# Kernel optimization log

Hardware: AMD Instinct MI355X
Metric: run time of the kernel (lower is better)

The kernel has to match this reference:

```python
import jax, jax.numpy as jnp
import numpy as np


def _conv1x1(x, W, b):
    # x: [B,C,H,W], W: [O,C], b: [O]  -> [B,O,H,W]
    return jnp.einsum('bchw,oc->bohw', x, W) + b[None, :, None, None]


def setup_inputs() -> dict:
    key = jax.random.key(0)
    ks = jax.random.split(key, 8)
    B, C, H, W = 16, 512, 48, 48
    d = C // 8
    scale = 0.02
    return {
        'feat_map': jax.random.normal(ks[0], (B, C, H, W), dtype=jnp.float32),
        'Wq': jax.random.normal(ks[1], (d, C), dtype=jnp.float32) * scale,
        'bq': jax.random.normal(ks[2], (d,), dtype=jnp.float32) * scale,
        'Wk': jax.random.normal(ks[3], (d, C), dtype=jnp.float32) * scale,
        'bk': jax.random.normal(ks[4], (d,), dtype=jnp.float32) * scale,
        'Wv': jax.random.normal(ks[5], (C, C), dtype=jnp.float32) * scale,
        'bv': jax.random.normal(ks[6], (C,), dtype=jnp.float32) * scale,
        'gamma': jnp.ones((1,), dtype=jnp.float32),
    }


def reference(feat_map, Wq, bq, Wk, bk, Wv, bv, gamma):
    # SAModule (DANet spatial attention):
    #   q = conv1(x) -> [B, d, HW] -> permute [B, HW, d]
    #   k = conv2(x) -> [B, d, HW]
    #   attn = softmax(q @ k, axis=-1)            # [B, HW, HW]
    #   v = conv3(x) -> [B, C, HW]
    #   out = v @ attn^T -> [B, C, H, W]
    #   y = gamma * out + x
    B, C, H, W = feat_map.shape
    HW = H * W
    q = _conv1x1(feat_map, Wq, bq).reshape(B, -1, HW).transpose(0, 2, 1)  # [B,HW,d]
    k = _conv1x1(feat_map, Wk, bk).reshape(B, -1, HW)                     # [B,d,HW]
    attn = jax.nn.softmax(jnp.einsum('bnd,bdm->bnm', q, k), axis=-1)      # [B,HW,HW]
    v = _conv1x1(feat_map, Wv, bv).reshape(B, C, HW)                      # [B,C,HW]
    out = jnp.einsum('bcm,bnm->bcn', v, attn).reshape(B, C, H, W)
    return gamma * out + feat_map
```

## Files before the change

kernel.cpp:

```cpp
#include <hip/hip_runtime.h>

typedef __bf16 bf16x8 __attribute__((ext_vector_type(8)));
typedef __bf16 bf16x4 __attribute__((ext_vector_type(4)));
typedef float  f32x4  __attribute__((ext_vector_type(4)));

constexpr int kHW = 2304;
constexpr int kC  = 512;

#if __has_builtin(__builtin_amdgcn_exp2f)
#define EXP2(x) __builtin_amdgcn_exp2f(x)
#else
#define EXP2(x) exp2f(x)
#endif

__device__ __forceinline__ void dma16(const __bf16* g, __bf16* l) {
    __builtin_amdgcn_global_load_lds(
        (const volatile __attribute__((address_space(1))) void*)g,
        (volatile __attribute__((address_space(3))) void*)l, 16, 0, 0);
}

__global__ void pack_weights(const float* __restrict__ Wq, const float* __restrict__ Wk,
                             const float* __restrict__ Wv, __bf16* __restrict__ Wqk2,
                             __bf16* __restrict__ Wvb2) {
    int idx = blockIdx.x * 256 + threadIdx.x;
    int o = idx >> 9, k = idx & 511, kb = k >> 6, kr = k & 63;
    if (idx < 64 * 512) {
        Wqk2[((size_t)kb * 128 + o) * 72 + kr]      = (__bf16)Wq[idx];
        Wqk2[((size_t)kb * 128 + 64 + o) * 72 + kr] = (__bf16)Wk[idx];
    }
    if (idx < 512 * 512)
        Wvb2[((size_t)kb * 512 + o) * 72 + kr] = (__bf16)Wv[idx];
}

__global__ void pack_x(const float* __restrict__ x, __bf16* __restrict__ XT2) {
    __shared__ __bf16 tile[64][65];
    int n0 = blockIdx.x * 64, kblk = blockIdx.y, b = blockIdx.z;
    int c0 = kblk * 64;
    int t = threadIdx.x;
    const float* xb = x + (size_t)b * kC * kHW;
#pragma unroll
    for (int rep = 0; rep < 16; ++rep) {
        int c_loc = rep * 4 + (t >> 6);
        int n_loc = t & 63;
        tile[c_loc][n_loc] = (__bf16)xb[(size_t)(c0 + c_loc) * kHW + n0 + n_loc];
    }
    __syncthreads();
    __bf16* dst = XT2 + ((size_t)b * 8 + kblk) * kHW * 72;
#pragma unroll
    for (int rep = 0; rep < 2; ++rep) {
        int item = rep * 256 + t;
        int n_loc = item >> 3, chunk = item & 7;
        bf16x8 v;
#pragma unroll
        for (int j = 0; j < 8; ++j) v[j] = tile[chunk * 8 + j][n_loc];
        *(bf16x8*)(dst + (size_t)(n0 + n_loc) * 72 + chunk * 8) = v;
    }
}

__global__ __launch_bounds__(256) void qkv_gemm(const __bf16* __restrict__ XT2,
                                                const __bf16* __restrict__ Wqk2,
                                                const __bf16* __restrict__ Wvb2,
                                                const float* __restrict__ bq,
                                                const float* __restrict__ bk,
                                                const float* __restrict__ bv,
                                                __bf16* __restrict__ qbuf,
                                                __bf16* __restrict__ kbuf,
                                                __bf16* __restrict__ vbuf2) {
    __shared__ __align__(16) __bf16 A_lds[128 * 72];
    __shared__ __align__(16) __bf16 B_lds[128 * 72];
    int r0 = blockIdx.x * 128, type = blockIdx.y, b = blockIdx.z;
    int t = threadIdx.x, wave = t >> 6, lane = t & 63, quad = lane >> 4, l16 = lane & 15;

    f32x4 acc[8][2];
#pragma unroll
    for (int i = 0; i < 8; ++i)
#pragma unroll
        for (int j = 0; j < 2; ++j) acc[i][j] = (f32x4){0.f, 0.f, 0.f, 0.f};

    for (int kb = 0; kb < 8; ++kb) {
        const __bf16* Asrc;
        const __bf16* Bsrc;
        if (type == 0) {
            Asrc = XT2 + (((size_t)b * 8 + kb) * kHW + r0) * 72;
            Bsrc = Wqk2 + (size_t)kb * 128 * 72;
        } else {
            Asrc = Wvb2 + ((size_t)kb * 512 + (type - 1) * 128) * 72;
            Bsrc = XT2 + (((size_t)b * 8 + kb) * kHW + r0) * 72;
        }
        __syncthreads();
        for (int ch = wave; ch < 18; ch += 4) {
            dma16(Asrc + ch * 512 + lane * 8, &A_lds[ch * 512]);
            dma16(Bsrc + ch * 512 + lane * 8, &B_lds[ch * 512]);
        }
        __syncthreads();
#pragma unroll
        for (int dk = 0; dk < 2; ++dk) {
            bf16x8 bfr[2];
#pragma unroll
            for (int ct = 0; ct < 2; ++ct)
                bfr[ct] = *(const bf16x8*)(&B_lds[(wave * 32 + ct * 16 + l16) * 72 + dk * 32 + quad * 8]);
#pragma unroll
            for (int rt = 0; rt < 8; ++rt) {
                bf16x8 a = *(const bf16x8*)(&A_lds[(rt * 16 + l16) * 72 + dk * 32 + quad * 8]);
#pragma unroll
                for (int ct = 0; ct < 2; ++ct)
                    acc[rt][ct] = __builtin_amdgcn_mfma_f32_16x16x32_bf16(a, bfr[ct], acc[rt][ct], 0, 0, 0);
            }
        }
    }

    if (type == 0) {
        constexpr float kLog2e = 1.4426950408889634f;
#pragma unroll
        for (int ct = 0; ct < 2; ++ct) {
            int o = wave * 32 + ct * 16 + l16;
            float bias = (o < 64) ? bq[o] : bk[o - 64];
            float scale = (o < 64) ? kLog2e : 1.0f;
#pragma unroll
            for (int rt = 0; rt < 8; ++rt)
#pragma unroll
                for (int r = 0; r < 4; ++r) {
                    int n = r0 + rt * 16 + quad * 4 + r;
                    __bf16 val = (__bf16)((acc[rt][ct][r] + bias) * scale);
                    if (o < 64) {
                        qbuf[((size_t)b * kHW + n) * 64 + o] = val;
                    } else {
                        int d = o - 64;
                        int dsw = (((d >> 3) ^ (n & 7)) << 3) | (d & 7);
                        kbuf[(((size_t)b * 72 + (n >> 5)) * 32 + (n & 31)) * 64 + dsw] = val;
                    }
                }
        }
    } else {
#pragma unroll
        for (int rt = 0; rt < 8; ++rt)
#pragma unroll
            for (int r = 0; r < 4; ++r) {
                int c = (type - 1) * 128 + rt * 16 + quad * 4 + r;
                float bias = bv[c];
#pragma unroll
                for (int ct = 0; ct < 2; ++ct) {
                    int m = r0 + wave * 32 + ct * 16 + l16;
                    vbuf2[(((size_t)b * 72 + (m >> 5)) * 512 + c) * 40 + (m & 31)] = (__bf16)(acc[rt][ct][r] + bias);
                }
            }
    }
}

__global__ __launch_bounds__(256, 4) void attn_kernel(const __bf16* __restrict__ qbuf,
                                                      const __bf16* __restrict__ kbuf,
                                                      const __bf16* __restrict__ vbuf2,
                                                      const float* __restrict__ x,
                                                      const float* __restrict__ gamma,
                                                      float* __restrict__ out) {
    __shared__ __align__(16) __bf16 K_lds[2][32 * 64];
    __shared__ __align__(16) __bf16 V_lds[2][128 * 40];
    __shared__ __align__(16) __bf16 P_lds[128 * 40];
    __shared__ float rs_lds[128];

    int n0 = blockIdx.x * 128, c0 = blockIdx.y * 128, b = blockIdx.z;
    int t = threadIdx.x, wave = t >> 6, lane = t & 63, quad = lane >> 4, l16 = lane & 15;
    const __bf16* q_b    = qbuf + (size_t)b * kHW * 64;
    const __bf16* k_base = kbuf + (size_t)b * 72 * 32 * 64;

    bf16x8 aq[2][2];
#pragma unroll
    for (int rt2 = 0; rt2 < 2; ++rt2)
#pragma unroll
        for (int dk = 0; dk < 2; ++dk)
            aq[rt2][dk] = *(const bf16x8*)(q_b + (size_t)(n0 + wave * 32 + rt2 * 16 + l16) * 64 + dk * 32 + quad * 8);

    f32x4 acc[2][8];
#pragma unroll
    for (int i = 0; i < 2; ++i)
#pragma unroll
        for (int j = 0; j < 8; ++j) acc[i][j] = (f32x4){0.f, 0.f, 0.f, 0.f};
    float rsum[2] = {0.f, 0.f};
    bf16x8 pf[2];

    auto issue_K = [&](int i, int buf) {
        const __bf16* ks = k_base + (size_t)i * 32 * 64;
        dma16(ks + wave * 512 + lane * 8, &K_lds[buf][wave * 512]);
    };
    auto issue_V = [&](int i, int buf) {
        const __bf16* vs = vbuf2 + (((size_t)b * 72 + i) * 512 + c0) * 40;
        for (int ch = wave; ch < 10; ch += 4)
            dma16(vs + ch * 512 + lane * 8, &V_lds[buf][ch * 512]);
    };
    auto qk_phase = [&](int j) {
        int kb_ = j & 1;
        __bf16* prow = &P_lds[(wave * 32 + l16) * 40 + quad * 4];
#pragma unroll
        for (int mt = 0; mt < 2; ++mt) {
            int row = mt * 16 + l16;
            int sw = (row & 7) << 3;
            bf16x8 kf0 = *(const bf16x8*)(&K_lds[kb_][row * 64 + ((quad * 8) ^ sw)]);
            bf16x8 kf1 = *(const bf16x8*)(&K_lds[kb_][row * 64 + ((32 + quad * 8) ^ sw)]);
#pragma unroll
            for (int rt2 = 0; rt2 < 2; ++rt2) {
                f32x4 s = (f32x4){0.f, 0.f, 0.f, 0.f};
                s = __builtin_amdgcn_mfma_f32_16x16x32_bf16(kf0, aq[rt2][0], s, 0, 0, 0);
                s = __builtin_amdgcn_mfma_f32_16x16x32_bf16(kf1, aq[rt2][1], s, 0, 0, 0);
                bf16x4 pv;
                float part = 0.f;
#pragma unroll
                for (int r = 0; r < 4; ++r) {
                    pv[r] = (__bf16)EXP2(s[r]);
                    part += (float)pv[r];
                }
                rsum[rt2] += part;
                *(bf16x4*)(prow + rt2 * 16 * 40 + mt * 16) = pv;
            }
        }
        pf[0] = *(const bf16x8*)(&P_lds[(wave * 32 + l16) * 40 + quad * 8]);
        pf[1] = *(const bf16x8*)(&P_lds[(wave * 32 + 16 + l16) * 40 + quad * 8]);
    };

    issue_K(0, 0);
    issue_V(0, 0);
    issue_K(1, 1);
    __syncthreads();
    qk_phase(0);

    for (int i = 0; i < 72; ++i) {
        __syncthreads();
        if (i + 2 < 72) issue_K(i + 2, i & 1);
        if (i + 1 < 72) issue_V(i + 1, (i + 1) & 1);

        __builtin_amdgcn_s_setprio(1);
#pragma unroll
        for (int ct = 0; ct < 8; ++ct) {
            bf16x8 vf = *(const bf16x8*)(&V_lds[i & 1][(ct * 16 + l16) * 40 + quad * 8]);
            acc[0][ct] = __builtin_amdgcn_mfma_f32_16x16x32_bf16(pf[0], vf, acc[0][ct], 0, 0, 0);
            acc[1][ct] = __builtin_amdgcn_mfma_f32_16x16x32_bf16(pf[1], vf, acc[1][ct], 0, 0, 0);
        }
        __builtin_amdgcn_s_setprio(0);

        if (i + 1 < 72) qk_phase(i + 1);
    }

#pragma unroll
    for (int rt2 = 0; rt2 < 2; ++rt2) {
        float v = rsum[rt2];
        v += __shfl_xor(v, 16);
        v += __shfl_xor(v, 32);
        if (quad == 0) rs_lds[wave * 32 + rt2 * 16 + l16] = v;
    }
    __syncthreads();

    float g = gamma[0];
    const float* x_b = x + (size_t)b * kC * kHW;
    float* out_b = out + (size_t)b * kC * kHW;
#pragma unroll
    for (int rt2 = 0; rt2 < 2; ++rt2) {
        float inv[4];
#pragma unroll
        for (int r = 0; r < 4; ++r) inv[r] = 1.f / rs_lds[wave * 32 + rt2 * 16 + quad * 4 + r];
#pragma unroll
        for (int ct = 0; ct < 8; ++ct) {
            int c = c0 + ct * 16 + l16;
            size_t base = (size_t)c * kHW + n0 + wave * 32 + rt2 * 16 + quad * 4;
            f32x4 xin = *(const f32x4*)(x_b + base);
            f32x4 y;
#pragma unroll
            for (int r = 0; r < 4; ++r) y[r] = g * acc[rt2][ct][r] * inv[r] + xin[r];
            *(f32x4*)(out_b + base) = y;
        }
    }
}

extern "C" void kernel_launch(void* const* d_in, const int* in_sizes, int n_in,
                              void* d_out, int out_size, void* d_ws, size_t ws_size,
                              hipStream_t stream) {
    const float* x     = (const float*)d_in[0];
    const float* Wq    = (const float*)d_in[1];
    const float* bq    = (const float*)d_in[2];
    const float* Wk    = (const float*)d_in[3];
    const float* bk    = (const float*)d_in[4];
    const float* Wv    = (const float*)d_in[5];
    const float* bv    = (const float*)d_in[6];
    const float* gamma = (const float*)d_in[7];
    float* out = (float*)d_out;

    char* ws = (char*)d_ws;
    __bf16* XT2   = (__bf16*)(ws);
    __bf16* Wqk2  = (__bf16*)(ws + 42467328);
    __bf16* Wvb2  = (__bf16*)(ws + 42614784);
    __bf16* qbuf  = (__bf16*)(ws + 43204608);
    __bf16* kbuf  = (__bf16*)(ws + 47923200);
    __bf16* vbuf2 = (__bf16*)(ws + 52641792);

    hipLaunchKernelGGL(pack_weights, dim3(1024), dim3(256), 0, stream, Wq, Wk, Wv, Wqk2, Wvb2);
    hipLaunchKernelGGL(pack_x, dim3(36, 8, 16), dim3(256), 0, stream, x, XT2);
    hipLaunchKernelGGL(qkv_gemm, dim3(18, 5, 16), dim3(256), 0, stream,
                       XT2, Wqk2, Wvb2, bq, bk, bv, qbuf, kbuf, vbuf2);
    hipLaunchKernelGGL(attn_kernel, dim3(18, 4, 16), dim3(256), 0, stream,
                       qbuf, kbuf, vbuf2, x, gamma, out);
}
```

Measured before the change: 380.8 us.

## Use two waves per attention block, each owning 64 query rows

The attention kernel now runs with 128 threads (2 waves) per block instead of 4. Each wave covers 64 query rows, so every V fragment read from LDS feeds four MFMAs instead of two, and K fragments are likewise reused across four row tiles. The exp row-sum now accumulates the fp32 value rather than the bf16-rounded one. The trade is fewer waves per block, more accumulator registers per wave (acc grows to 4x8 vectors), and the DMA work split over fewer waves, which may lower occupancy and latency hiding.

Result: slower. 418.5 us (+9.9%).

```diff
diff --git a/kernel.cpp b/kernel.cpp
--- a/kernel.cpp
+++ b/kernel.cpp
@@ -147,7 +147,7 @@
     }
 }
 
-__global__ __launch_bounds__(256, 4) void attn_kernel(const __bf16* __restrict__ qbuf,
+__global__ __launch_bounds__(128, 2) void attn_kernel(const __bf16* __restrict__ qbuf,
                                                       const __bf16* __restrict__ kbuf,
                                                       const __bf16* __restrict__ vbuf2,
                                                       const float* __restrict__ x,
@@ -163,33 +163,34 @@
     const __bf16* q_b    = qbuf + (size_t)b * kHW * 64;
     const __bf16* k_base = kbuf + (size_t)b * 72 * 32 * 64;
 
-    bf16x8 aq[2][2];
-#pragma unroll
-    for (int rt2 = 0; rt2 < 2; ++rt2)
+    bf16x8 aq[4][2];
+#pragma unroll
+    for (int rt = 0; rt < 4; ++rt)
 #pragma unroll
         for (int dk = 0; dk < 2; ++dk)
-            aq[rt2][dk] = *(const bf16x8*)(q_b + (size_t)(n0 + wave * 32 + rt2 * 16 + l16) * 64 + dk * 32 + quad * 8);
-
-    f32x4 acc[2][8];
-#pragma unroll
-    for (int i = 0; i < 2; ++i)
+            aq[rt][dk] = *(const bf16x8*)(q_b + (size_t)(n0 + wave * 64 + rt * 16 + l16) * 64 + dk * 32 + quad * 8);
+
+    f32x4 acc[4][8];
+#pragma unroll
+    for (int i = 0; i < 4; ++i)
 #pragma unroll
         for (int j = 0; j < 8; ++j) acc[i][j] = (f32x4){0.f, 0.f, 0.f, 0.f};
-    float rsum[2] = {0.f, 0.f};
-    bf16x8 pf[2];
+    float rsum[4] = {0.f, 0.f, 0.f, 0.f};
+    bf16x8 pf[4];
 
     auto issue_K = [&](int i, int buf) {
         const __bf16* ks = k_base + (size_t)i * 32 * 64;
-        dma16(ks + wave * 512 + lane * 8, &K_lds[buf][wave * 512]);
+        for (int ch = wave; ch < 4; ch += 2)
+            dma16(ks + ch * 512 + lane * 8, &K_lds[buf][ch * 512]);
     };
     auto issue_V = [&](int i, int buf) {
         const __bf16* vs = vbuf2 + (((size_t)b * 72 + i) * 512 + c0) * 40;
-        for (int ch = wave; ch < 10; ch += 4)
+        for (int ch = wave; ch < 10; ch += 2)
             dma16(vs + ch * 512 + lane * 8, &V_lds[buf][ch * 512]);
     };
     auto qk_phase = [&](int j) {
         int kb_ = j & 1;
-        __bf16* prow = &P_lds[(wave * 32 + l16) * 40 + quad * 4];
+        __bf16* prow = &P_lds[(wave * 64 + l16) * 40 + quad * 4];
 #pragma unroll
         for (int mt = 0; mt < 2; ++mt) {
             int row = mt * 16 + l16;
@@ -197,23 +198,25 @@
             bf16x8 kf0 = *(const bf16x8*)(&K_lds[kb_][row * 64 + ((quad * 8) ^ sw)]);
             bf16x8 kf1 = *(const bf16x8*)(&K_lds[kb_][row * 64 + ((32 + quad * 8) ^ sw)]);
 #pragma unroll
-            for (int rt2 = 0; rt2 < 2; ++rt2) {
+            for (int rt = 0; rt < 4; ++rt) {
                 f32x4 s = (f32x4){0.f, 0.f, 0.f, 0.f};
-                s = __builtin_amdgcn_mfma_f32_16x16x32_bf16(kf0, aq[rt2][0], s, 0, 0, 0);
-                s = __builtin_amdgcn_mfma_f32_16x16x32_bf16(kf1, aq[rt2][1], s, 0, 0, 0);
+                s = __builtin_amdgcn_mfma_f32_16x16x32_bf16(kf0, aq[rt][0], s, 0, 0, 0);
+                s = __builtin_amdgcn_mfma_f32_16x16x32_bf16(kf1, aq[rt][1], s, 0, 0, 0);
                 bf16x4 pv;
                 float part = 0.f;
 #pragma unroll
                 for (int r = 0; r < 4; ++r) {
-                    pv[r] = (__bf16)EXP2(s[r]);
-                    part += (float)pv[r];
+                    float e = EXP2(s[r]);
+                    pv[r] = (__bf16)e;
+                    part += e;
                 }
-                rsum[rt2] += part;
-                *(bf16x4*)(prow + rt2 * 16 * 40 + mt * 16) = pv;
+                rsum[rt] += part;
+                *(bf16x4*)(prow + rt * 16 * 40 + mt * 16) = pv;
             }
         }
-        pf[0] = *(const bf16x8*)(&P_lds[(wave * 32 + l16) * 40 + quad * 8]);
-        pf[1] = *(const bf16x8*)(&P_lds[(wave * 32 + 16 + l16) * 40 + quad * 8]);
+#pragma unroll
+        for (int rt = 0; rt < 4; ++rt)
+            pf[rt] = *(const bf16x8*)(&P_lds[(wave * 64 + rt * 16 + l16) * 40 + quad * 8]);
     };
 
     issue_K(0, 0);
@@ -233,6 +236,8 @@
             bf16x8 vf = *(const bf16x8*)(&V_lds[i & 1][(ct * 16 + l16) * 40 + quad * 8]);
             acc[0][ct] = __builtin_amdgcn_mfma_f32_16x16x32_bf16(pf[0], vf, acc[0][ct], 0, 0, 0);
             acc[1][ct] = __builtin_amdgcn_mfma_f32_16x16x32_bf16(pf[1], vf, acc[1][ct], 0, 0, 0);
+            acc[2][ct] = __builtin_amdgcn_mfma_f32_16x16x32_bf16(pf[2], vf, acc[2][ct], 0, 0, 0);
+            acc[3][ct] = __builtin_amdgcn_mfma_f32_16x16x32_bf16(pf[3], vf, acc[3][ct], 0, 0, 0);
         }
         __builtin_amdgcn_s_setprio(0);
 
@@ -240,11 +245,11 @@
     }
 
 #pragma unroll
-    for (int rt2 = 0; rt2 < 2; ++rt2) {
-        float v = rsum[rt2];
+    for (int rt = 0; rt < 4; ++rt) {
+        float v = rsum[rt];
         v += __shfl_xor(v, 16);
         v += __shfl_xor(v, 32);
-        if (quad == 0) rs_lds[wave * 32 + rt2 * 16 + l16] = v;
+        if (quad == 0) rs_lds[wave * 64 + rt * 16 + l16] = v;
     }
     __syncthreads();
 
@@ -252,18 +257,18 @@
     const float* x_b = x + (size_t)b * kC * kHW;
     float* out_b = out + (size_t)b * kC * kHW;
 #pragma unroll
-    for (int rt2 = 0; rt2 < 2; ++rt2) {
+    for (int rt = 0; rt < 4; ++rt) {
         float inv[4];
 #pragma unroll
-        for (int r = 0; r < 4; ++r) inv[r] = 1.f / rs_lds[wave * 32 + rt2 * 16 + quad * 4 + r];
+        for (int r = 0; r < 4; ++r) inv[r] = 1.f / rs_lds[wave * 64 + rt * 16 + quad * 4 + r];
 #pragma unroll
         for (int ct = 0; ct < 8; ++ct) {
             int c = c0 + ct * 16 + l16;
-            size_t base = (size_t)c * kHW + n0 + wave * 32 + rt2 * 16 + quad * 4;
+            size_t base = (size_t)c * kHW + n0 + wave * 64 + rt * 16 + quad * 4;
             f32x4 xin = *(const f32x4*)(x_b + base);
             f32x4 y;
 #pragma unroll
-            for (int r = 0; r < 4; ++r) y[r] = g * acc[rt2][ct][r] * inv[r] + xin[r];
+            for (int r = 0; r < 4; ++r) y[r] = g * acc[rt][ct][r] * inv[r] + xin[r];
             *(f32x4*)(out_b + base) = y;
         }
     }
@@ -294,6 +299,6 @@
     hipLaunchKernelGGL(pack_x, dim3(36, 8, 16), dim3(256), 0, stream, x, XT2);
     hipLaunchKernelGGL(qkv_gemm, dim3(18, 5, 16), dim3(256), 0, stream,
                        XT2, Wqk2, Wvb2, bq, bk, bv, qbuf, kbuf, vbuf2);
-    hipLaunchKernelGGL(attn_kernel, dim3(18, 4, 16), dim3(256), 0, stream,
+    hipLaunchKernelGGL(attn_kernel, dim3(18, 4, 16), dim3(128), 0, stream,
                        qbuf, kbuf, vbuf2, x, gamma, out);
 }
```
